# Optimization experiments

Hardware: AMD Instinct MI355X
Metric: run time of the kernel (lower is better)

The kernel has to match this reference:

```python
import jax, jax.numpy as jnp
import numpy as np

B, N, D_MODEL, H = 2, 512, 256, 8
DH, DS, DE = 8, 8, 8          # hyperbolic / spherical / euclidean component dims
HEAD = D_MODEL // H           # 32
HALF = HEAD // 2              # 16 rope frequencies
KAPPA_S = 1.0                 # spherical curvature
EPS = 1e-6


def setup_inputs() -> dict:
    key = jax.random.key(0)
    ks = jax.random.split(key, 10)
    h = jax.random.normal(ks[0], (B, N, D_MODEL), jnp.float32)
    # manifold coords: hyperbolic part inside Poincare ball, spherical part on unit sphere
    xh = 0.3 * jnp.tanh(jax.random.normal(ks[1], (B, N, DH), jnp.float32))
    xs_raw = jax.random.normal(ks[2], (B, N, DS), jnp.float32)
    xs = xs_raw / jnp.linalg.norm(xs_raw, axis=-1, keepdims=True)
    xe = jax.random.normal(ks[3], (B, N, DE), jnp.float32)
    x = jnp.concatenate([xh, xs, xe], axis=-1)
    def lin(k):
        return 0.05 * jax.random.normal(k, (D_MODEL, D_MODEL), jnp.float32)
    inp = dict(
        h=h, x=x,
        Wq=lin(ks[4]), bq=jnp.zeros((D_MODEL,), jnp.float32),
        Wk=lin(ks[5]), bk=jnp.zeros((D_MODEL,), jnp.float32),
        Wv=lin(ks[6]), bv=jnp.zeros((D_MODEL,), jnp.float32),
        Wo=lin(ks[7]), bo=jnp.zeros((D_MODEL,), jnp.float32),
        w_kernel=jnp.ones((H, 3), jnp.float32),   # torch init: ones(num_heads, num_comp)
        beta=jnp.ones((H,), jnp.float32),
        edge_bias=0.1 * jax.random.normal(ks[8], (B, 1, N, N), jnp.float32),
        node_mask=jnp.ones((B, N), bool),
    )
    return inp


def _pairwise_geometry(x):
    """Returns dh (B,N,N), sdot (B,N,N), de2 (B,N,N), dist (B,N,N)."""
    xh, xs, xe = x[..., :DH], x[..., DH:DH + DS], x[..., DH + DS:]
    # hyperbolic: Poincare-ball distance arccosh(1 + 2|a-b|^2 / ((1-|a|^2)(1-|b|^2)))
    dh2_num = jnp.sum((xh[:, :, None, :] - xh[:, None, :, :]) ** 2, -1)
    one_m = 1.0 - jnp.sum(xh * xh, -1)                               # (B,N)
    arg = 1.0 + 2.0 * dh2_num / (one_m[:, :, None] * one_m[:, None, :])
    dh = jnp.arccosh(jnp.maximum(arg, 1.0 + EPS))
    # spherical: arccos of dot (unit vectors); raw dot kept for the kernel term
    sdot = jnp.einsum('bnd,bmd->bnm', xs, xs)
    ds = jnp.arccos(jnp.clip(sdot, -1.0 + EPS, 1.0 - EPS)) / np.sqrt(KAPPA_S)
    # euclidean: squared distance (kernel uses -d^2; product dist uses d^2)
    de2 = jnp.sum((xe[:, :, None, :] - xe[:, None, :, :]) ** 2, -1)
    dist = jnp.sqrt(dh * dh + ds * ds + de2)
    return dh, sdot, de2, dist


def reference(h, x, Wq, bq, Wk, bk, Wv, bv, Wo, bo, w_kernel, beta, edge_bias, node_mask):
    scale = 1.0 / np.sqrt(HEAD)
    rope_freq = jnp.exp(-np.log(10000.0) * jnp.arange(HALF, dtype=jnp.float32) / HALF)

    def heads(t):  # (B,N,D) -> (B,H,N,head)
        return t.reshape(B, N, H, HEAD).transpose(0, 2, 1, 3)

    Q = heads(h @ Wq.T + bq)
    K = heads(h @ Wk.T + bk)
    V = heads(h @ Wv.T + bv)

    dh, sdot, de2, dist = _pairwise_geometry(x)

    # M-RoPE: rotate Q by pairwise angle theta_ij = omega * d_M(x_i, x_j)
    theta = dist[..., None] * rope_freq                  # (B,N,N,half)
    cos_t = jnp.cos(theta)[:, None]                      # (B,1,N,N,half)
    sin_t = jnp.sin(theta)[:, None]
    q1, q2 = Q[..., 0::2], Q[..., 1::2]                  # (B,H,N,half)
    k1, k2 = K[..., 0::2], K[..., 1::2]
    qk_same = q1[:, :, :, None, :] * k1[:, :, None, :, :] + q2[:, :, :, None, :] * k2[:, :, None, :, :]
    qk_cross = q1[:, :, :, None, :] * k2[:, :, None, :, :] - q2[:, :, :, None, :] * k1[:, :, None, :, :]
    attn = (cos_t * qk_same + sin_t * qk_cross).sum(-1) * scale   # (B,H,N,N)

    # geodesic kernel bias: per-component kernels [H:-d_H, S:k*a.b, E:-|a-b|^2]
    kernel_stack = jnp.stack([-dh, KAPPA_S * sdot, -de2], axis=-1)  # (B,N,N,3)
    geo = jnp.einsum('hc,bnmc->bhnm', w_kernel, kernel_stack)
    attn = attn + beta[None, :, None, None] * geo + edge_bias

    attn = jnp.where(node_mask[:, None, None, :], attn, -jnp.inf)
    p = jax.nn.softmax(attn, axis=-1)
    out = jnp.einsum('bhnm,bhmd->bhnd', p, V).transpose(0, 2, 1, 3).reshape(B, N, D_MODEL)
    return out @ Wo.T + bo
```

## Files before the change

### kernel.cpp

```cpp
#include <hip/hip_runtime.h>

#define N_TOK 512
#define NH 8

__global__ __launch_bounds__(256) void gemm_qkv_kernel(
    const float* __restrict__ A,
    const float* __restrict__ Wq, const float* __restrict__ Wk, const float* __restrict__ Wv,
    const float* __restrict__ bq, const float* __restrict__ bk, const float* __restrict__ bv,
    float* __restrict__ Qb, float* __restrict__ Kb, float* __restrict__ Vb)
{
    const float* W; const float* bias; float* C;
    if (blockIdx.z == 0)      { W = Wq; bias = bq; C = Qb; }
    else if (blockIdx.z == 1) { W = Wk; bias = bk; C = Kb; }
    else                      { W = Wv; bias = bv; C = Vb; }

    __shared__ float As[32 * 34];
    __shared__ float Ws[32 * 34];
    const int t = threadIdx.x;
    const int tx = t & 15, ty = t >> 4;
    const int m0 = blockIdx.y * 32, n0 = blockIdx.x * 32;
    const int srow = t >> 3, sc4 = (t & 7) * 4;

    float acc[2][2] = {{0.f, 0.f}, {0.f, 0.f}};

    for (int k0 = 0; k0 < 256; k0 += 32) {
        __syncthreads();
        {
            float4 a = *(const float4*)&A[(m0 + srow) * 256 + k0 + sc4];
            As[(sc4 + 0) * 34 + srow] = a.x; As[(sc4 + 1) * 34 + srow] = a.y;
            As[(sc4 + 2) * 34 + srow] = a.z; As[(sc4 + 3) * 34 + srow] = a.w;
            float4 w = *(const float4*)&W[(n0 + srow) * 256 + k0 + sc4];
            Ws[(sc4 + 0) * 34 + srow] = w.x; Ws[(sc4 + 1) * 34 + srow] = w.y;
            Ws[(sc4 + 2) * 34 + srow] = w.z; Ws[(sc4 + 3) * 34 + srow] = w.w;
        }
        __syncthreads();
        #pragma unroll
        for (int kk = 0; kk < 32; ++kk) {
            float a0 = As[kk * 34 + ty * 2], a1 = As[kk * 34 + ty * 2 + 1];
            float w0 = Ws[kk * 34 + tx * 2], w1 = Ws[kk * 34 + tx * 2 + 1];
            acc[0][0] += a0 * w0; acc[0][1] += a0 * w1;
            acc[1][0] += a1 * w0; acc[1][1] += a1 * w1;
        }
    }
    float b0 = bias[n0 + tx * 2], b1 = bias[n0 + tx * 2 + 1];
    #pragma unroll
    for (int i = 0; i < 2; ++i) {
        float2 o; o.x = acc[i][0] + b0; o.y = acc[i][1] + b1;
        *(float2*)&C[(m0 + ty * 2 + i) * 256 + n0 + tx * 2] = o;
    }
}

__global__ __launch_bounds__(512, 4) void attn_kernel(
    const float* __restrict__ Q, const float* __restrict__ K, const float* __restrict__ V,
    const float* __restrict__ x, const float* __restrict__ wker, const float* __restrict__ beta,
    const float* __restrict__ eb, float* __restrict__ num, float* __restrict__ den)
{
    const int i0 = blockIdx.x * 4;
    const int jh = blockIdx.y;
    const int b  = blockIdx.z;
    const int jbase = jh * 256;
    const int t = threadIdx.x;
    const int h = t >> 6;
    const int lane = t & 63;

    __shared__ float  Qs[4 * 256];
    __shared__ float  xls[256 * 25];
    __shared__ float2 csn[16][4][64];
    __shared__ float  es[4][NH][64];
    __shared__ float  gdh[4][64], gsd[4][64], gde[4][64];
    __shared__ float  xih[4][8], xis[4][8], xie[4][8], onemi[4];
    __shared__ float  freqs[16];

    if (t < 256) ((float4*)Qs)[t] = ((const float4*)(Q + (size_t)(b * N_TOK + i0) * 256))[t];
    {
        const float4* xsrc = (const float4*)(x + (size_t)(b * N_TOK + jbase) * 24);
        for (int r = t; r < 1536; r += 512) {
            float4 v = xsrc[r];
            int row = r / 6, c = (r % 6) * 4;
            float* dst = &xls[row * 25 + c];
            dst[0] = v.x; dst[1] = v.y; dst[2] = v.z; dst[3] = v.w;
        }
    }
    if (t < 16) freqs[t] = __expf(-0.5756462732485115f * (float)t);
    if (t < 4) {
        const float* xp = x + (size_t)(b * N_TOK + i0 + t) * 24;
        float s2 = 0.f;
        #pragma unroll
        for (int k = 0; k < 8; ++k) { float v = xp[k]; xih[t][k] = v; s2 += v * v; }
        onemi[t] = 1.0f - s2;
        #pragma unroll
        for (int k = 0; k < 8; ++k) xis[t][k] = xp[8 + k];
        #pragma unroll
        for (int k = 0; k < 8; ++k) xie[t][k] = xp[16 + k];
    }
    const float wk0 = wker[h * 3 + 0], wk1 = wker[h * 3 + 1], wk2 = wker[h * 3 + 2];
    const float bet = beta[h];
    const float scale = 0.17677669529663687f;

    float dsum[4] = {0.f, 0.f, 0.f, 0.f};
    float acc[2]  = {0.f, 0.f};

    const int gii  = t >> 7;
    const int gsub = (t >> 6) & 1;
    const int d    = lane & 31;
    const int isub = lane >> 5;

    for (int tile = 0; tile < 4; ++tile) {
        const int j0l = tile * 64;
        const int j0g = jbase + j0l;
        __syncthreads();
        {
            const int jj = lane;
            const float* xr = &xls[(j0l + jj) * 25];
            float dh2 = 0.f, oj = 0.f, sd = 0.f, de2 = 0.f;
            #pragma unroll
            for (int k = 0; k < 8; ++k) { float xj = xr[k]; float dd = xih[gii][k] - xj; dh2 += dd * dd; oj += xj * xj; }
            #pragma unroll
            for (int k = 0; k < 8; ++k) sd += xis[gii][k] * xr[8 + k];
            #pragma unroll
            for (int k = 0; k < 8; ++k) { float dd = xie[gii][k] - xr[16 + k]; de2 += dd * dd; }
            float arg = 1.0f + 2.0f * dh2 / (onemi[gii] * (1.0f - oj));
            arg = fmaxf(arg, 1.0f + 1e-6f);
            float dh = __logf(arg + sqrtf(arg * arg - 1.0f));
            float sdc = fminf(fmaxf(sd, -1.0f + 1e-6f), 1.0f - 1e-6f);
            float dsp = acosf(sdc);
            float dist = sqrtf(dh * dh + dsp * dsp + de2);
            if (gsub == 0) { gdh[gii][jj] = dh; gsd[gii][jj] = sd; gde[gii][jj] = de2; }
            #pragma unroll
            for (int k2 = 0; k2 < 8; ++k2) {
                int f = gsub * 8 + k2;
                float sv, cv;
                __sincosf(dist * freqs[f], &sv, &cv);
                csn[f][gii][jj] = make_float2(cv, sv);
            }
        }
        __syncthreads();
        {
            float s[4] = {0.f, 0.f, 0.f, 0.f};
            const float* kr = K + (size_t)(b * N_TOK + j0g + lane) * 256 + h * 32;
            #pragma unroll
            for (int g = 0; g < 4; ++g) {
                float4 ka = ((const float4*)kr)[g * 2 + 0];
                float4 kb = ((const float4*)kr)[g * 2 + 1];
                float kkv[8] = {ka.x, ka.y, ka.z, ka.w, kb.x, kb.y, kb.z, kb.w};
                #pragma unroll
                for (int ii = 0; ii < 4; ++ii) {
                    const float4* qp = (const float4*)&Qs[ii * 256 + h * 32 + g * 8];
                    float4 qa = qp[0], qb = qp[1];
                    float qv[8] = {qa.x, qa.y, qa.z, qa.w, qb.x, qb.y, qb.z, qb.w};
                    #pragma unroll
                    for (int f2 = 0; f2 < 4; ++f2) {
                        float2 cspair = csn[g * 4 + f2][ii][lane];
                        float q1 = qv[f2 * 2], q2 = qv[f2 * 2 + 1];
                        float k1 = kkv[f2 * 2], k2 = kkv[f2 * 2 + 1];
                        float same  = q1 * k1 + q2 * k2;
                        float cross = q1 * k2 - q2 * k1;
                        s[ii] += cspair.x * same + cspair.y * cross;
                    }
                }
            }
            #pragma unroll
            for (int ii = 0; ii < 4; ++ii) {
                float sv = s[ii] * scale
                         + bet * (wk1 * gsd[ii][lane] - wk0 * gdh[ii][lane] - wk2 * gde[ii][lane])
                         + eb[((size_t)b * N_TOK + i0 + ii) * N_TOK + j0g + lane];
                float e = __expf(sv);
                dsum[ii] += e;
                es[ii][h][lane] = e;
            }
        }
        __syncthreads();
        {
            const float* vcol = V + (size_t)(b * N_TOK + j0g) * 256 + h * 32 + d;
            #pragma unroll
            for (int j4 = 0; j4 < 16; ++j4) {
                float v0 = vcol[(j4 * 4 + 0) * 256];
                float v1 = vcol[(j4 * 4 + 1) * 256];
                float v2 = vcol[(j4 * 4 + 2) * 256];
                float v3 = vcol[(j4 * 4 + 3) * 256];
                #pragma unroll
                for (int ip = 0; ip < 2; ++ip) {
                    float4 e4 = *(const float4*)&es[isub * 2 + ip][h][j4 * 4];
                    acc[ip] += e4.x * v0 + e4.y * v1 + e4.z * v2 + e4.w * v3;
                }
            }
        }
    }
    #pragma unroll
    for (int ii = 0; ii < 4; ++ii) {
        float v = dsum[ii];
        v += __shfl_xor(v, 1);  v += __shfl_xor(v, 2);  v += __shfl_xor(v, 4);
        v += __shfl_xor(v, 8);  v += __shfl_xor(v, 16); v += __shfl_xor(v, 32);
        dsum[ii] = v;
    }
    float* nump = num + (size_t)jh * 262144;
    float* denp = den + (size_t)jh * 8192;
    if (lane == 0) {
        #pragma unroll
        for (int ii = 0; ii < 4; ++ii)
            denp[((size_t)b * N_TOK + i0 + ii) * 8 + h] = dsum[ii];
    }
    #pragma unroll
    for (int ip = 0; ip < 2; ++ip)
        nump[((size_t)b * N_TOK + i0 + isub * 2 + ip) * 256 + h * 32 + d] = acc[ip];
}

__global__ __launch_bounds__(256) void gemm_out_kernel(
    const float* __restrict__ num, const float* __restrict__ den,
    const float* __restrict__ Wo, const float* __restrict__ bo, float* __restrict__ out)
{
    __shared__ float As[32 * 34];
    __shared__ float Ws[32 * 34];
    const int t = threadIdx.x;
    const int tx = t & 15, ty = t >> 4;
    const int m0 = blockIdx.y * 32, n0 = blockIdx.x * 32;
    const int srow = t >> 3, sc4 = (t & 7) * 4;

    float acc[2][2] = {{0.f, 0.f}, {0.f, 0.f}};

    for (int k0 = 0; k0 < 256; k0 += 32) {
        __syncthreads();
        {
            int m = m0 + srow, kk0 = k0 + sc4;
            float4 a0 = *(const float4*)&num[m * 256 + kk0];
            float4 a1 = *(const float4*)&num[262144 + m * 256 + kk0];
            int hh = k0 >> 5;
            float dsum = den[m * 8 + hh] + den[8192 + m * 8 + hh];
            float inv = 1.0f / dsum;
            As[(sc4 + 0) * 34 + srow] = (a0.x + a1.x) * inv;
            As[(sc4 + 1) * 34 + srow] = (a0.y + a1.y) * inv;
            As[(sc4 + 2) * 34 + srow] = (a0.z + a1.z) * inv;
            As[(sc4 + 3) * 34 + srow] = (a0.w + a1.w) * inv;
            float4 w = *(const float4*)&Wo[(n0 + srow) * 256 + kk0];
            Ws[(sc4 + 0) * 34 + srow] = w.x; Ws[(sc4 + 1) * 34 + srow] = w.y;
            Ws[(sc4 + 2) * 34 + srow] = w.z; Ws[(sc4 + 3) * 34 + srow] = w.w;
        }
        __syncthreads();
        #pragma unroll
        for (int kk = 0; kk < 32; ++kk) {
            float a0 = As[kk * 34 + ty * 2], a1 = As[kk * 34 + ty * 2 + 1];
            float w0 = Ws[kk * 34 + tx * 2], w1 = Ws[kk * 34 + tx * 2 + 1];
            acc[0][0] += a0 * w0; acc[0][1] += a0 * w1;
            acc[1][0] += a1 * w0; acc[1][1] += a1 * w1;
        }
    }
    float b0 = bo[n0 + tx * 2], b1 = bo[n0 + tx * 2 + 1];
    #pragma unroll
    for (int i = 0; i < 2; ++i) {
        float2 o; o.x = acc[i][0] + b0; o.y = acc[i][1] + b1;
        *(float2*)&out[(m0 + ty * 2 + i) * 256 + n0 + tx * 2] = o;
    }
}

extern "C" void kernel_launch(void* const* d_in, const int* in_sizes, int n_in,
                              void* d_out, int out_size, void* d_ws, size_t ws_size,
                              hipStream_t stream) {
    const float* hin  = (const float*)d_in[0];
    const float* x    = (const float*)d_in[1];
    const float* Wq   = (const float*)d_in[2];
    const float* bq   = (const float*)d_in[3];
    const float* Wk   = (const float*)d_in[4];
    const float* bk   = (const float*)d_in[5];
    const float* Wv   = (const float*)d_in[6];
    const float* bv   = (const float*)d_in[7];
    const float* Wo   = (const float*)d_in[8];
    const float* bo   = (const float*)d_in[9];
    const float* wker = (const float*)d_in[10];
    const float* beta = (const float*)d_in[11];
    const float* eb   = (const float*)d_in[12];
    float* out = (float*)d_out;
    float* w   = (float*)d_ws;

    float* Qb  = w;
    float* Kb  = w + 262144;
    float* Vb  = w + 524288;
    float* num = w + 786432;
    float* den = w + 1310720;

    hipLaunchKernelGGL(gemm_qkv_kernel, dim3(8, 32, 3), dim3(256), 0, stream,
                       hin, Wq, Wk, Wv, bq, bk, bv, Qb, Kb, Vb);
    hipLaunchKernelGGL(attn_kernel, dim3(128, 2, 2), dim3(512), 0, stream,
                       Qb, Kb, Vb, x, wker, beta, eb, num, den);
    hipLaunchKernelGGL(gemm_out_kernel, dim3(8, 32), dim3(256), 0, stream,
                       num, den, Wo, bo, out);
}
```

Measured before the change: 146.5 us.

## Use bf16 MFMA for projections and restructure attention to full-row blocks

Replaces both fp32 SIMT GEMMs with per-wave 16x16x32 bf16 MFMA tiles that convert fp32 inputs to bf16 on the fly. The attention kernel now processes two query rows over all 512 keys per block, which removes the split-key partial num/den buffers and lets the output GEMM skip the merge and normalisation. It also overlaps the geometry for the next tile with the PV accumulation and reads x, Q and V directly from global memory. The bf16 conversion lowers GEMM precision, and the smaller query tile means K and V are re-read from global memory more often.

```diff
diff --git a/kernel.cpp b/kernel.cpp
--- a/kernel.cpp
+++ b/kernel.cpp
@@ -3,253 +3,228 @@
 #define N_TOK 512
 #define NH 8
 
-__global__ __launch_bounds__(256) void gemm_qkv_kernel(
+typedef __attribute__((ext_vector_type(8))) short short8;
+typedef __attribute__((ext_vector_type(4))) float f32x4;
+
+__device__ __forceinline__ unsigned short f2bf(float f) {
+    union { float f; unsigned u; } v; v.f = f;
+    unsigned r = (v.u + 0x7FFF + ((v.u >> 16) & 1)) >> 16;
+    return (unsigned short)r;
+}
+__device__ __forceinline__ short8 frag_from_f32(const float* p) {
+    float4 a = *(const float4*)p;
+    float4 b = *(const float4*)(p + 4);
+    union { short8 s; unsigned short u[8]; } fr;
+    fr.u[0] = f2bf(a.x); fr.u[1] = f2bf(a.y); fr.u[2] = f2bf(a.z); fr.u[3] = f2bf(a.w);
+    fr.u[4] = f2bf(b.x); fr.u[5] = f2bf(b.y); fr.u[6] = f2bf(b.z); fr.u[7] = f2bf(b.w);
+    return fr.s;
+}
+
+__global__ __launch_bounds__(256) void gemm_qkv_mfma(
     const float* __restrict__ A,
     const float* __restrict__ Wq, const float* __restrict__ Wk, const float* __restrict__ Wv,
     const float* __restrict__ bq, const float* __restrict__ bk, const float* __restrict__ bv,
     float* __restrict__ Qb, float* __restrict__ Kb, float* __restrict__ Vb)
 {
-    const float* W; const float* bias; float* C;
-    if (blockIdx.z == 0)      { W = Wq; bias = bq; C = Qb; }
-    else if (blockIdx.z == 1) { W = Wk; bias = bk; C = Kb; }
-    else                      { W = Wv; bias = bv; C = Vb; }
-
-    __shared__ float As[32 * 34];
-    __shared__ float Ws[32 * 34];
-    const int t = threadIdx.x;
-    const int tx = t & 15, ty = t >> 4;
-    const int m0 = blockIdx.y * 32, n0 = blockIdx.x * 32;
-    const int srow = t >> 3, sc4 = (t & 7) * 4;
-
-    float acc[2][2] = {{0.f, 0.f}, {0.f, 0.f}};
-
-    for (int k0 = 0; k0 < 256; k0 += 32) {
-        __syncthreads();
-        {
-            float4 a = *(const float4*)&A[(m0 + srow) * 256 + k0 + sc4];
-            As[(sc4 + 0) * 34 + srow] = a.x; As[(sc4 + 1) * 34 + srow] = a.y;
-            As[(sc4 + 2) * 34 + srow] = a.z; As[(sc4 + 3) * 34 + srow] = a.w;
-            float4 w = *(const float4*)&W[(n0 + srow) * 256 + k0 + sc4];
-            Ws[(sc4 + 0) * 34 + srow] = w.x; Ws[(sc4 + 1) * 34 + srow] = w.y;
-            Ws[(sc4 + 2) * 34 + srow] = w.z; Ws[(sc4 + 3) * 34 + srow] = w.w;
-        }
-        __syncthreads();
-        #pragma unroll
-        for (int kk = 0; kk < 32; ++kk) {
-            float a0 = As[kk * 34 + ty * 2], a1 = As[kk * 34 + ty * 2 + 1];
-            float w0 = Ws[kk * 34 + tx * 2], w1 = Ws[kk * 34 + tx * 2 + 1];
-            acc[0][0] += a0 * w0; acc[0][1] += a0 * w1;
-            acc[1][0] += a1 * w0; acc[1][1] += a1 * w1;
-        }
-    }
-    float b0 = bias[n0 + tx * 2], b1 = bias[n0 + tx * 2 + 1];
-    #pragma unroll
-    for (int i = 0; i < 2; ++i) {
-        float2 o; o.x = acc[i][0] + b0; o.y = acc[i][1] + b1;
-        *(float2*)&C[(m0 + ty * 2 + i) * 256 + n0 + tx * 2] = o;
-    }
+    const int tile = blockIdx.x * 4 + (threadIdx.x >> 6);
+    const int lane = threadIdx.x & 63;
+    const int z = tile >> 10;
+    const int rem = tile & 1023;
+    const int m0 = (rem >> 4) * 16, n0 = (rem & 15) * 16;
+    const float* W    = (z == 0) ? Wq : (z == 1) ? Wk : Wv;
+    const float* bias = (z == 0) ? bq : (z == 1) ? bk : bv;
+    float*       C    = (z == 0) ? Qb : (z == 1) ? Kb : Vb;
+
+    const int mrow = lane & 15, kq = lane >> 4;
+    const float* ap = A + (m0 + mrow) * 256 + kq * 8;
+    const float* wp = W + (n0 + mrow) * 256 + kq * 8;
+
+    f32x4 acc = {0.f, 0.f, 0.f, 0.f};
+    #pragma unroll
+    for (int k0 = 0; k0 < 8; ++k0) {
+        short8 af = frag_from_f32(ap + k0 * 32);
+        short8 bf = frag_from_f32(wp + k0 * 32);
+        acc = __builtin_amdgcn_mfma_f32_16x16x32_bf16(af, bf, acc, 0, 0, 0);
+    }
+    const int col = lane & 15, rowb = (lane >> 4) * 4;
+    float bsv = bias[n0 + col];
+    #pragma unroll
+    for (int r = 0; r < 4; ++r)
+        C[(m0 + rowb + r) * 256 + n0 + col] = acc[r] + bsv;
 }
 
 __global__ __launch_bounds__(512, 4) void attn_kernel(
     const float* __restrict__ Q, const float* __restrict__ K, const float* __restrict__ V,
     const float* __restrict__ x, const float* __restrict__ wker, const float* __restrict__ beta,
-    const float* __restrict__ eb, float* __restrict__ num, float* __restrict__ den)
+    const float* __restrict__ eb, float* __restrict__ Ao)
 {
-    const int i0 = blockIdx.x * 4;
-    const int jh = blockIdx.y;
-    const int b  = blockIdx.z;
-    const int jbase = jh * 256;
-    const int t = threadIdx.x;
-    const int h = t >> 6;
+    const int i0 = blockIdx.x * 2;
+    const int b  = blockIdx.y;
+    const int t  = threadIdx.x;
     const int lane = t & 63;
-
-    __shared__ float  Qs[4 * 256];
-    __shared__ float  xls[256 * 25];
-    __shared__ float2 csn[16][4][64];
-    __shared__ float  es[4][NH][64];
-    __shared__ float  gdh[4][64], gsd[4][64], gde[4][64];
-    __shared__ float  xih[4][8], xis[4][8], xie[4][8], onemi[4];
-    __shared__ float  freqs[16];
-
-    if (t < 256) ((float4*)Qs)[t] = ((const float4*)(Q + (size_t)(b * N_TOK + i0) * 256))[t];
-    {
-        const float4* xsrc = (const float4*)(x + (size_t)(b * N_TOK + jbase) * 24);
-        for (int r = t; r < 1536; r += 512) {
-            float4 v = xsrc[r];
-            int row = r / 6, c = (r % 6) * 4;
-            float* dst = &xls[row * 25 + c];
-            dst[0] = v.x; dst[1] = v.y; dst[2] = v.z; dst[3] = v.w;
-        }
-    }
-    if (t < 16) freqs[t] = __expf(-0.5756462732485115f * (float)t);
-    if (t < 4) {
-        const float* xp = x + (size_t)(b * N_TOK + i0 + t) * 24;
-        float s2 = 0.f;
-        #pragma unroll
-        for (int k = 0; k < 8; ++k) { float v = xp[k]; xih[t][k] = v; s2 += v * v; }
-        onemi[t] = 1.0f - s2;
-        #pragma unroll
-        for (int k = 0; k < 8; ++k) xis[t][k] = xp[8 + k];
-        #pragma unroll
-        for (int k = 0; k < 8; ++k) xie[t][k] = xp[16 + k];
-    }
-    const float wk0 = wker[h * 3 + 0], wk1 = wker[h * 3 + 1], wk2 = wker[h * 3 + 2];
-    const float bet = beta[h];
+    const int hs = __builtin_amdgcn_readfirstlane(t >> 6);
+
+    __shared__ float2 csn[16][2][64];
+    __shared__ float  es[2][NH][64];
+    __shared__ float  gdh[2][64], gsd[2][64], gde[2][64];
+
+    const int gii = __builtin_amdgcn_readfirstlane(t >> 8);
+    const int fq  = __builtin_amdgcn_readfirstlane((t >> 6) & 3);
+    float frq[4];
+    #pragma unroll
+    for (int r = 0; r < 4; ++r)
+        frq[r] = __expf(-0.5756462732485115f * (float)(fq * 4 + r));
+
+    const float* xi = x + (size_t)(b * N_TOK + i0 + gii) * 24;
+    float onemi = 1.0f;
+    #pragma unroll
+    for (int k = 0; k < 8; ++k) onemi -= xi[k] * xi[k];
+
+    const float wk0 = wker[hs * 3 + 0], wk1 = wker[hs * 3 + 1], wk2 = wker[hs * 3 + 2];
+    const float bet = beta[hs];
     const float scale = 0.17677669529663687f;
 
-    float dsum[4] = {0.f, 0.f, 0.f, 0.f};
-    float acc[2]  = {0.f, 0.f};
-
-    const int gii  = t >> 7;
-    const int gsub = (t >> 6) & 1;
-    const int d    = lane & 31;
-    const int isub = lane >> 5;
-
-    for (int tile = 0; tile < 4; ++tile) {
-        const int j0l = tile * 64;
-        const int j0g = jbase + j0l;
+    float dsum[2] = {0.f, 0.f};
+    float accv[2][4] = {{0.f,0.f,0.f,0.f},{0.f,0.f,0.f,0.f}};
+    const int d4 = lane >> 3, jo = lane & 7;
+
+    auto geom = [&](int tile) {
+        const int jj = lane;
+        const float* xr = x + (size_t)(b * N_TOK + tile * 64 + jj) * 24;
+        float4 x0 = *(const float4*)xr,        x1 = *(const float4*)(xr + 4);
+        float4 x2 = *(const float4*)(xr + 8),  x3 = *(const float4*)(xr + 12);
+        float4 x4 = *(const float4*)(xr + 16), x5 = *(const float4*)(xr + 20);
+        float xv[24] = {x0.x,x0.y,x0.z,x0.w, x1.x,x1.y,x1.z,x1.w,
+                        x2.x,x2.y,x2.z,x2.w, x3.x,x3.y,x3.z,x3.w,
+                        x4.x,x4.y,x4.z,x4.w, x5.x,x5.y,x5.z,x5.w};
+        float dh2 = 0.f, oj = 0.f, sd = 0.f, de2 = 0.f;
+        #pragma unroll
+        for (int k = 0; k < 8; ++k) { float xj = xv[k]; float d = xi[k] - xj; dh2 += d * d; oj += xj * xj; }
+        #pragma unroll
+        for (int k = 0; k < 8; ++k) sd += xi[8 + k] * xv[8 + k];
+        #pragma unroll
+        for (int k = 0; k < 8; ++k) { float d = xi[16 + k] - xv[16 + k]; de2 += d * d; }
+        float arg = 1.0f + 2.0f * dh2 / (onemi * (1.0f - oj));
+        arg = fmaxf(arg, 1.0f + 1e-6f);
+        float dh = __logf(arg + sqrtf(arg * arg - 1.0f));
+        float sdc = fminf(fmaxf(sd, -1.0f + 1e-6f), 1.0f - 1e-6f);
+        float dsp = acosf(sdc);
+        float dist = sqrtf(dh * dh + dsp * dsp + de2);
+        if (fq == 0) { gdh[gii][jj] = dh; gsd[gii][jj] = sd; gde[gii][jj] = de2; }
+        #pragma unroll
+        for (int r = 0; r < 4; ++r) {
+            float sv, cv;
+            __sincosf(dist * frq[r], &sv, &cv);
+            csn[fq * 4 + r][gii][jj] = make_float2(cv, sv);
+        }
+    };
+
+    geom(0);
+    __syncthreads();
+
+    for (int tile = 0; tile < 8; ++tile) {
+        {
+            float sb[2], dot[2] = {0.f, 0.f};
+            #pragma unroll
+            for (int ii = 0; ii < 2; ++ii)
+                sb[ii] = bet * (wk1 * gsd[ii][lane] - wk0 * gdh[ii][lane] - wk2 * gde[ii][lane])
+                       + eb[((size_t)b * N_TOK + i0 + ii) * N_TOK + tile * 64 + lane];
+            const float* kr = K + (size_t)(b * N_TOK + tile * 64 + lane) * 256 + hs * 32;
+            const float* q0 = Q + (size_t)(b * N_TOK + i0) * 256 + hs * 32;
+            const float* q1 = q0 + 256;
+            #pragma unroll
+            for (int g = 0; g < 4; ++g) {
+                float4 ka = ((const float4*)kr)[2 * g], kb = ((const float4*)kr)[2 * g + 1];
+                float kv[8] = {ka.x, ka.y, ka.z, ka.w, kb.x, kb.y, kb.z, kb.w};
+                #pragma unroll
+                for (int f2 = 0; f2 < 4; ++f2) {
+                    float2 c0 = csn[g * 4 + f2][0][lane];
+                    float2 c1 = csn[g * 4 + f2][1][lane];
+                    float k1v = kv[f2 * 2], k2v = kv[f2 * 2 + 1];
+                    float qa0 = q0[g * 8 + f2 * 2], qb0 = q0[g * 8 + f2 * 2 + 1];
+                    float qa1 = q1[g * 8 + f2 * 2], qb1 = q1[g * 8 + f2 * 2 + 1];
+                    dot[0] += c0.x * (qa0 * k1v + qb0 * k2v) + c0.y * (qa0 * k2v - qb0 * k1v);
+                    dot[1] += c1.x * (qa1 * k1v + qb1 * k2v) + c1.y * (qa1 * k2v - qb1 * k1v);
+                }
+            }
+            #pragma unroll
+            for (int ii = 0; ii < 2; ++ii) {
+                float e = __expf(dot[ii] * scale + sb[ii]);
+                dsum[ii] += e;
+                es[ii][hs][lane] = e;
+            }
+        }
         __syncthreads();
         {
-            const int jj = lane;
-            const float* xr = &xls[(j0l + jj) * 25];
-            float dh2 = 0.f, oj = 0.f, sd = 0.f, de2 = 0.f;
-            #pragma unroll
-            for (int k = 0; k < 8; ++k) { float xj = xr[k]; float dd = xih[gii][k] - xj; dh2 += dd * dd; oj += xj * xj; }
-            #pragma unroll
-            for (int k = 0; k < 8; ++k) sd += xis[gii][k] * xr[8 + k];
-            #pragma unroll
-            for (int k = 0; k < 8; ++k) { float dd = xie[gii][k] - xr[16 + k]; de2 += dd * dd; }
-            float arg = 1.0f + 2.0f * dh2 / (onemi[gii] * (1.0f - oj));
-            arg = fmaxf(arg, 1.0f + 1e-6f);
-            float dh = __logf(arg + sqrtf(arg * arg - 1.0f));
-            float sdc = fminf(fmaxf(sd, -1.0f + 1e-6f), 1.0f - 1e-6f);
-            float dsp = acosf(sdc);
-            float dist = sqrtf(dh * dh + dsp * dsp + de2);
-            if (gsub == 0) { gdh[gii][jj] = dh; gsd[gii][jj] = sd; gde[gii][jj] = de2; }
-            #pragma unroll
-            for (int k2 = 0; k2 < 8; ++k2) {
-                int f = gsub * 8 + k2;
-                float sv, cv;
-                __sincosf(dist * freqs[f], &sv, &cv);
-                csn[f][gii][jj] = make_float2(cv, sv);
+            float4 e0a = *(const float4*)&es[0][hs][jo * 8];
+            float4 e0b = *(const float4*)&es[0][hs][jo * 8 + 4];
+            float4 e1a = *(const float4*)&es[1][hs][jo * 8];
+            float4 e1b = *(const float4*)&es[1][hs][jo * 8 + 4];
+            float e0[8] = {e0a.x,e0a.y,e0a.z,e0a.w, e0b.x,e0b.y,e0b.z,e0b.w};
+            float e1[8] = {e1a.x,e1a.y,e1a.z,e1a.w, e1b.x,e1b.y,e1b.z,e1b.w};
+            const float* vb = V + (size_t)(b * N_TOK + tile * 64 + jo * 8) * 256 + hs * 32 + d4 * 4;
+            #pragma unroll
+            for (int jj = 0; jj < 8; ++jj) {
+                float4 v = *(const float4*)&vb[jj * 256];
+                accv[0][0] += e0[jj] * v.x; accv[0][1] += e0[jj] * v.y;
+                accv[0][2] += e0[jj] * v.z; accv[0][3] += e0[jj] * v.w;
+                accv[1][0] += e1[jj] * v.x; accv[1][1] += e1[jj] * v.y;
+                accv[1][2] += e1[jj] * v.z; accv[1][3] += e1[jj] * v.w;
             }
         }
+        if (tile < 7) geom(tile + 1);
         __syncthreads();
-        {
-            float s[4] = {0.f, 0.f, 0.f, 0.f};
-            const float* kr = K + (size_t)(b * N_TOK + j0g + lane) * 256 + h * 32;
-            #pragma unroll
-            for (int g = 0; g < 4; ++g) {
-                float4 ka = ((const float4*)kr)[g * 2 + 0];
-                float4 kb = ((const float4*)kr)[g * 2 + 1];
-                float kkv[8] = {ka.x, ka.y, ka.z, ka.w, kb.x, kb.y, kb.z, kb.w};
-                #pragma unroll
-                for (int ii = 0; ii < 4; ++ii) {
-                    const float4* qp = (const float4*)&Qs[ii * 256 + h * 32 + g * 8];
-                    float4 qa = qp[0], qb = qp[1];
-                    float qv[8] = {qa.x, qa.y, qa.z, qa.w, qb.x, qb.y, qb.z, qb.w};
-                    #pragma unroll
-                    for (int f2 = 0; f2 < 4; ++f2) {
-                        float2 cspair = csn[g * 4 + f2][ii][lane];
-                        float q1 = qv[f2 * 2], q2 = qv[f2 * 2 + 1];
-                        float k1 = kkv[f2 * 2], k2 = kkv[f2 * 2 + 1];
-                        float same  = q1 * k1 + q2 * k2;
-                        float cross = q1 * k2 - q2 * k1;
-                        s[ii] += cspair.x * same + cspair.y * cross;
-                    }
-                }
-            }
-            #pragma unroll
-            for (int ii = 0; ii < 4; ++ii) {
-                float sv = s[ii] * scale
-                         + bet * (wk1 * gsd[ii][lane] - wk0 * gdh[ii][lane] - wk2 * gde[ii][lane])
-                         + eb[((size_t)b * N_TOK + i0 + ii) * N_TOK + j0g + lane];
-                float e = __expf(sv);
-                dsum[ii] += e;
-                es[ii][h][lane] = e;
-            }
-        }
-        __syncthreads();
-        {
-            const float* vcol = V + (size_t)(b * N_TOK + j0g) * 256 + h * 32 + d;
-            #pragma unroll
-            for (int j4 = 0; j4 < 16; ++j4) {
-                float v0 = vcol[(j4 * 4 + 0) * 256];
-                float v1 = vcol[(j4 * 4 + 1) * 256];
-                float v2 = vcol[(j4 * 4 + 2) * 256];
-                float v3 = vcol[(j4 * 4 + 3) * 256];
-                #pragma unroll
-                for (int ip = 0; ip < 2; ++ip) {
-                    float4 e4 = *(const float4*)&es[isub * 2 + ip][h][j4 * 4];
-                    acc[ip] += e4.x * v0 + e4.y * v1 + e4.z * v2 + e4.w * v3;
-                }
-            }
-        }
-    }
-    #pragma unroll
-    for (int ii = 0; ii < 4; ++ii) {
+    }
+
+    #pragma unroll
+    for (int ii = 0; ii < 2; ++ii) {
         float v = dsum[ii];
         v += __shfl_xor(v, 1);  v += __shfl_xor(v, 2);  v += __shfl_xor(v, 4);
         v += __shfl_xor(v, 8);  v += __shfl_xor(v, 16); v += __shfl_xor(v, 32);
-        dsum[ii] = v;
-    }
-    float* nump = num + (size_t)jh * 262144;
-    float* denp = den + (size_t)jh * 8192;
-    if (lane == 0) {
-        #pragma unroll
-        for (int ii = 0; ii < 4; ++ii)
-            denp[((size_t)b * N_TOK + i0 + ii) * 8 + h] = dsum[ii];
-    }
-    #pragma unroll
-    for (int ip = 0; ip < 2; ++ip)
-        nump[((size_t)b * N_TOK + i0 + isub * 2 + ip) * 256 + h * 32 + d] = acc[ip];
-}
-
-__global__ __launch_bounds__(256) void gemm_out_kernel(
-    const float* __restrict__ num, const float* __restrict__ den,
-    const float* __restrict__ Wo, const float* __restrict__ bo, float* __restrict__ out)
+        dsum[ii] = 1.0f / v;
+    }
+    #pragma unroll
+    for (int ii = 0; ii < 2; ++ii)
+        #pragma unroll
+        for (int dd = 0; dd < 4; ++dd) {
+            float a = accv[ii][dd];
+            a += __shfl_xor(a, 1); a += __shfl_xor(a, 2); a += __shfl_xor(a, 4);
+            accv[ii][dd] = a;
+        }
+    if (jo == 0) {
+        #pragma unroll
+        for (int ii = 0; ii < 2; ++ii) {
+            float4 o;
+            o.x = accv[ii][0] * dsum[ii]; o.y = accv[ii][1] * dsum[ii];
+            o.z = accv[ii][2] * dsum[ii]; o.w = accv[ii][3] * dsum[ii];
+            *(float4*)&Ao[(size_t)(b * N_TOK + i0 + ii) * 256 + hs * 32 + d4 * 4] = o;
+        }
+    }
+}
+
+__global__ __launch_bounds__(256) void gemm_out_mfma(
+    const float* __restrict__ Ao, const float* __restrict__ Wo,
+    const float* __restrict__ bo, float* __restrict__ out)
 {
-    __shared__ float As[32 * 34];
-    __shared__ float Ws[32 * 34];
-    const int t = threadIdx.x;
-    const int tx = t & 15, ty = t >> 4;
-    const int m0 = blockIdx.y * 32, n0 = blockIdx.x * 32;
-    const int srow = t >> 3, sc4 = (t & 7) * 4;
-
-    float acc[2][2] = {{0.f, 0.f}, {0.f, 0.f}};
-
-    for (int k0 = 0; k0 < 256; k0 += 32) {
-        __syncthreads();
-        {
-            int m = m0 + srow, kk0 = k0 + sc4;
-            float4 a0 = *(const float4*)&num[m * 256 + kk0];
-            float4 a1 = *(const float4*)&num[262144 + m * 256 + kk0];
-            int hh = k0 >> 5;
-            float dsum = den[m * 8 + hh] + den[8192 + m * 8 + hh];
-            float inv = 1.0f / dsum;
-            As[(sc4 + 0) * 34 + srow] = (a0.x + a1.x) * inv;
-            As[(sc4 + 1) * 34 + srow] = (a0.y + a1.y) * inv;
-            As[(sc4 + 2) * 34 + srow] = (a0.z + a1.z) * inv;
-            As[(sc4 + 3) * 34 + srow] = (a0.w + a1.w) * inv;
-            float4 w = *(const float4*)&Wo[(n0 + srow) * 256 + kk0];
-            Ws[(sc4 + 0) * 34 + srow] = w.x; Ws[(sc4 + 1) * 34 + srow] = w.y;
-            Ws[(sc4 + 2) * 34 + srow] = w.z; Ws[(sc4 + 3) * 34 + srow] = w.w;
-        }
-        __syncthreads();
-        #pragma unroll
-        for (int kk = 0; kk < 32; ++kk) {
-            float a0 = As[kk * 34 + ty * 2], a1 = As[kk * 34 + ty * 2 + 1];
-            float w0 = Ws[kk * 34 + tx * 2], w1 = Ws[kk * 34 + tx * 2 + 1];
-            acc[0][0] += a0 * w0; acc[0][1] += a0 * w1;
-            acc[1][0] += a1 * w0; acc[1][1] += a1 * w1;
-        }
-    }
-    float b0 = bo[n0 + tx * 2], b1 = bo[n0 + tx * 2 + 1];
-    #pragma unroll
-    for (int i = 0; i < 2; ++i) {
-        float2 o; o.x = acc[i][0] + b0; o.y = acc[i][1] + b1;
-        *(float2*)&out[(m0 + ty * 2 + i) * 256 + n0 + tx * 2] = o;
-    }
+    const int tile = blockIdx.x * 4 + (threadIdx.x >> 6);
+    const int lane = threadIdx.x & 63;
+    const int m0 = (tile >> 4) * 16, n0 = (tile & 15) * 16;
+    const int mrow = lane & 15, kq = lane >> 4;
+    const float* ap = Ao + (m0 + mrow) * 256 + kq * 8;
+    const float* wp = Wo + (n0 + mrow) * 256 + kq * 8;
+
+    f32x4 acc = {0.f, 0.f, 0.f, 0.f};
+    #pragma unroll
+    for (int k0 = 0; k0 < 8; ++k0) {
+        short8 af = frag_from_f32(ap + k0 * 32);
+        short8 bf = frag_from_f32(wp + k0 * 32);
+        acc = __builtin_amdgcn_mfma_f32_16x16x32_bf16(af, bf, acc, 0, 0, 0);
+    }
+    const int col = lane & 15, rowb = (lane >> 4) * 4;
+    float bsv = bo[n0 + col];
+    #pragma unroll
+    for (int r = 0; r < 4; ++r)
+        out[(m0 + rowb + r) * 256 + n0 + col] = acc[r] + bsv;
 }
 
 extern "C" void kernel_launch(void* const* d_in, const int* in_sizes, int n_in,
@@ -271,16 +246,15 @@
     float* out = (float*)d_out;
     float* w   = (float*)d_ws;
 
-    float* Qb  = w;
-    float* Kb  = w + 262144;
-    float* Vb  = w + 524288;
-    float* num = w + 786432;
-    float* den = w + 1310720;
-
-    hipLaunchKernelGGL(gemm_qkv_kernel, dim3(8, 32, 3), dim3(256), 0, stream,
+    float* Qb = w;
+    float* Kb = w + 262144;
+    float* Vb = w + 524288;
+    float* Ao = w + 786432;
+
+    hipLaunchKernelGGL(gemm_qkv_mfma, dim3(768), dim3(256), 0, stream,
                        hin, Wq, Wk, Wv, bq, bk, bv, Qb, Kb, Vb);
-    hipLaunchKernelGGL(attn_kernel, dim3(128, 2, 2), dim3(512), 0, stream,
-                       Qb, Kb, Vb, x, wker, beta, eb, num, den);
-    hipLaunchKernelGGL(gemm_out_kernel, dim3(8, 32), dim3(256), 0, stream,
-                       num, den, Wo, bo, out);
-}
+    hipLaunchKernelGGL(attn_kernel, dim3(256, 2), dim3(512), 0, stream,
+                       Qb, Kb, Vb, x, wker, beta, eb, Ao);
+    hipLaunchKernelGGL(gemm_out_mfma, dim3(256), dim3(256), 0, stream,
+                       Ao, Wo, bo, out);
+}
```

After: 178.3 us. 21.7% more time.
